# Performance work log

Hardware: AMD Instinct MI355X
Metric: run time of the kernel (lower is better)

Reference implementation:

```python
import jax, jax.numpy as jnp
import numpy as np

BATCH, SEQ, H_IN, N_STATE, H_OUT = 16, 4096, 128, 256, 128
RMIN, RMAX, MAX_PHASE = 0.9, 1.0, 6.283


def setup_inputs() -> dict:
    key = jax.random.key(0)
    ks = jax.random.split(key, 9)
    u = jax.random.normal(ks[0], (BATCH, SEQ, H_IN), jnp.float32)
    # LRU exponential parameterization init (matches torch __init__)
    u1 = jax.random.uniform(ks[1], (N_STATE,), jnp.float32)
    u2 = jax.random.uniform(ks[2], (N_STATE,), jnp.float32)
    nu_log = jnp.log(-0.5 * jnp.log(u1 * (RMAX + RMIN) * (RMAX - RMIN) + RMIN ** 2))
    theta_log = jnp.log(MAX_PHASE * u2)
    lam_abs = jnp.exp(-jnp.exp(nu_log))
    gamma_log = jnp.log(jnp.sqrt(1.0 - lam_abs ** 2))
    s2in = np.sqrt(2.0 * H_IN).astype(np.float32)
    B_re = jax.random.normal(ks[3], (N_STATE, H_IN), jnp.float32) / s2in
    B_im = jax.random.normal(ks[4], (N_STATE, H_IN), jnp.float32) / s2in
    sst = np.sqrt(float(N_STATE)).astype(np.float32)
    C_re = jax.random.normal(ks[5], (H_OUT, N_STATE), jnp.float32) / sst
    C_im = jax.random.normal(ks[6], (H_OUT, N_STATE), jnp.float32) / sst
    D = jax.random.normal(ks[7], (H_OUT, H_IN), jnp.float32) / np.sqrt(float(H_IN)).astype(np.float32)
    return dict(u=u, nu_log=nu_log, theta_log=theta_log, gamma_log=gamma_log,
                B_re=B_re, B_im=B_im, C_re=C_re, C_im=C_im, D=D)


def _combine(a, b):
    # complex affine composition: (l, x) o (l', x') -> (l*l', l'*x + x')
    l1r, l1i, x1r, x1i = a
    l2r, l2i, x2r, x2i = b
    lr = l1r * l2r - l1i * l2i
    li = l1r * l2i + l1i * l2r
    xr = l2r * x1r - l2i * x1i + x2r
    xi = l2r * x1i + l2i * x1r + x2i
    return (lr, li, xr, xi)


def reference(u, nu_log, theta_log, gamma_log, B_re, B_im, C_re, C_im, D):
    lam_mod = jnp.exp(-jnp.exp(nu_log))          # |lambda|, [N]
    th = jnp.exp(theta_log)
    lam_re = lam_mod * jnp.cos(th)
    lam_im = lam_mod * jnp.sin(th)
    gammas = jnp.exp(gamma_log)                  # [N]
    # input projection Bu_t = gamma * (B @ u_t), complex -> real/imag parts
    Bu_re = jnp.einsum('blh,nh->bln', u, B_re) * gammas  # [B,L,N]
    Bu_im = jnp.einsum('blh,nh->bln', u, B_im) * gammas
    Bsz, L, N = Bu_re.shape
    lr = jnp.broadcast_to(lam_re, (Bsz, L, N))
    li = jnp.broadcast_to(lam_im, (Bsz, L, N))
    # parallel scan of x_t = lambda * x_{t-1} + Bu_t, x0 = 0
    _, _, xr, xi = jax.lax.associative_scan(_combine, (lr, li, Bu_re, Bu_im), axis=1)
    zero = jnp.zeros((Bsz, 1, N), u.dtype)
    pre_re = jnp.concatenate([zero, xr[:, :-1]], axis=1)  # states[:, :-1]
    pre_im = jnp.concatenate([zero, xi[:, :-1]], axis=1)
    # y_t = Re(C x_{t-1}) + D u_t
    y = (jnp.einsum('bln,on->blo', pre_re, C_re)
         - jnp.einsum('bln,on->blo', pre_im, C_im)
         + jnp.einsum('blh,oh->blo', u, D))
    return y
```

## Files before the change

kernel.cpp:

```cpp
#include <hip/hip_runtime.h>
#include <math.h>

#define BATCH 16
#define SEQ   4096
#define HIN   128
#define NST   256
#define HOUT  128
#define CL    32
#define NC    (SEQ/CL)
#define ROWS  (BATCH*SEQ)
#define KTOT  640

typedef __attribute__((ext_vector_type(8))) short short8;
typedef __attribute__((ext_vector_type(4))) float f32x4;

__device__ inline unsigned short f2bf(float f) {
  union { float f; unsigned u; } v; v.f = f;
  unsigned r = v.u + 0x7FFFu + ((v.u >> 16) & 1u);
  return (unsigned short)(r >> 16);
}
__device__ inline float bf2f(unsigned short s) {
  union { unsigned u; float f; } v; v.u = ((unsigned)s) << 16;
  return v.f;
}
__device__ inline float bits2f(unsigned u) {
  union { unsigned u; float f; } v; v.u = u; return v.f;
}

__global__ __launch_bounds__(256) void k_prep(
    const float* __restrict__ nu_log, const float* __restrict__ theta_log,
    const float* __restrict__ gamma_log,
    const float* __restrict__ Bre, const float* __restrict__ Bim,
    const float* __restrict__ Cre, const float* __restrict__ Cim,
    const float* __restrict__ Dm,
    float* __restrict__ lamre, float* __restrict__ lamim,
    unsigned short* __restrict__ Wb, unsigned short* __restrict__ W2) {
  int idx = blockIdx.x*256 + threadIdx.x;
  if (idx < NST) {
    float lm = expf(-expf(nu_log[idx]));
    float th = expf(theta_log[idx]);
    lamre[idx] = lm * cosf(th);
    lamim[idx] = lm * sinf(th);
  }
  if (idx < 512*HIN) {
    int r = idx >> 7, h = idx & 127;
    int g = r >> 7;
    int w = r & 127;
    int n = g*64 + (w & 63);
    float gm = expf(gamma_log[n]);
    float v = (w < 64) ? Bre[n*HIN + h] : Bim[n*HIN + h];
    Wb[idx] = f2bf(gm * v);
  }
  if (idx < HOUT*KTOT) {
    int o = idx / KTOT, k = idx - o*KTOT;
    float v;
    if (k < 512) {
      int g = k >> 7, kk = k & 127;
      int n = g*64 + (kk & 63);
      v = (kk < 64) ? Cre[o*NST + n] : -Cim[o*NST + n];
    } else {
      v = Dm[o*HIN + (k - 512)];
    }
    W2[idx] = f2bf(v);
  }
}

union SharedK1 {
  unsigned short B[128][72];
  unsigned short stgb[2][32][136];
};
__global__ __launch_bounds__(256, 4) void k_bu(
    const float* __restrict__ u, const unsigned short* __restrict__ Wb,
    const float* __restrict__ lamre, const float* __restrict__ lamim,
    float* __restrict__ S_re, float* __restrict__ S_im) {
  __shared__ unsigned short Asl[64][136];
  __shared__ SharedK1 sh;
  int tid = threadIdx.x;
  int row0 = blockIdx.x * 64;
  int wid = tid >> 6, lane = tid & 63;
  int lm = lane & 15, lq = lane >> 4;
  int m0 = wid * 16;
  int b = row0 >> 12;
  int cbase = (row0 & 4095) >> 5;
#pragma unroll
  for (int cc = 0; cc < 4; ++cc) {
    int ch = cc*256 + tid;
    int r = ch >> 4, h0 = (ch & 15) * 8;
    const float* src = u + (size_t)(row0 + r)*HIN + h0;
    float4 v0 = *(const float4*)src;
    float4 v1 = *(const float4*)(src + 4);
    unsigned short o[8];
    o[0]=f2bf(v0.x); o[1]=f2bf(v0.y); o[2]=f2bf(v0.z); o[3]=f2bf(v0.w);
    o[4]=f2bf(v1.x); o[5]=f2bf(v1.y); o[6]=f2bf(v1.z); o[7]=f2bf(v1.w);
    *(short8*)&Asl[r][h0] = *(const short8*)o;
  }
  for (int g = 0; g < 4; ++g) {
    f32x4 accB[8];
#pragma unroll
    for (int j = 0; j < 8; ++j) accB[j] = (f32x4)0.f;
    for (int kh = 0; kh < 2; ++kh) {
      __syncthreads();
#pragma unroll
      for (int cc = 0; cc < 4; ++cc) {
        int ch = cc*256 + tid;
        int r = ch >> 3, h0 = (ch & 7) * 8;
        *(short8*)&sh.B[r][h0] = *(const short8*)&Wb[(size_t)(g*128 + r)*HIN + kh*64 + h0];
      }
      __syncthreads();
#pragma unroll
      for (int ks2 = 0; ks2 < 2; ++ks2) {
        int k0 = (kh*2 + ks2)*32 + lq*8;
        short8 a = *(const short8*)&Asl[m0 + lm][k0];
#pragma unroll
        for (int j = 0; j < 8; ++j) {
          short8 bb = *(const short8*)&sh.B[j*16 + lm][k0 - kh*64];
          accB[j] = __builtin_amdgcn_mfma_f32_16x16x32_bf16(a, bb, accB[j], 0, 0, 0);
        }
      }
    }
    __syncthreads();
#pragma unroll
    for (int j = 0; j < 8; ++j)
#pragma unroll
      for (int r = 0; r < 4; ++r) {
        int row = m0 + lq*4 + r;
        sh.stgb[row >> 5][row & 31][j*16 + lm] = f2bf(accB[j][r]);
      }
    __syncthreads();
    if (tid < 128) {
      int buf = tid >> 6, nl = tid & 63;
      int ng = g*64 + nl;
      float lr = lamre[ng], li = lamim[ng];
      float rr[CL], ri[CL];
#pragma unroll
      for (int t = 0; t < CL; ++t) {
        rr[t] = bf2f(sh.stgb[buf][t][nl]);
        ri[t] = bf2f(sh.stgb[buf][t][64 + nl]);
      }
      float sr = 0.f, si = 0.f;
#pragma unroll
      for (int t = 0; t < CL; ++t) {
        float nr = lr*sr - li*si + rr[t];
        float ni = lr*si + li*sr + ri[t];
        sr = nr; si = ni;
      }
      int c = cbase + buf;
      int idx = (b*NC + c)*NST + ng;
      S_re[idx] = sr; S_im[idx] = si;
    }
  }
}

__global__ __launch_bounds__(64) void k_scan(
    const float* __restrict__ S_re, const float* __restrict__ S_im,
    const float* __restrict__ lamre, const float* __restrict__ lamim,
    unsigned* __restrict__ X0Pk) {
  int b = blockIdx.x >> 2;
  int n = (blockIdx.x & 3) * 64 + threadIdx.x;
  float ar = lamre[n], ai = lamim[n];
#pragma unroll
  for (int s = 0; s < 5; ++s) { float nr = ar*ar - ai*ai, ni = 2.f*ar*ai; ar = nr; ai = ni; }
  const float* Sr = S_re + (size_t)b*NC*NST + n;
  const float* Si = S_im + (size_t)b*NC*NST + n;
  unsigned* Xp = X0Pk + (size_t)b*NC*NST + n;
  float Are[16], Aim[16], Bre[16], Bim[16];
#pragma unroll
  for (int cc = 0; cc < 16; ++cc) { Are[cc] = Sr[cc*NST]; Aim[cc] = Si[cc*NST]; }
  float xr = 0.f, xi = 0.f;
#pragma unroll
  for (int seg = 0; seg < 8; ++seg) {
    if (seg < 7) {
      const float* pr = Sr + (size_t)(seg+1)*16*NST;
      const float* pi = Si + (size_t)(seg+1)*16*NST;
      if (seg & 1) {
#pragma unroll
        for (int cc = 0; cc < 16; ++cc) { Are[cc] = pr[cc*NST]; Aim[cc] = pi[cc*NST]; }
      } else {
#pragma unroll
        for (int cc = 0; cc < 16; ++cc) { Bre[cc] = pr[cc*NST]; Bim[cc] = pi[cc*NST]; }
      }
    }
#pragma unroll
    for (int cc = 0; cc < 16; ++cc) {
      Xp[(size_t)(seg*16 + cc)*NST] = ((unsigned)f2bf(xi) << 16) | (unsigned)f2bf(xr);
      float cr = (seg & 1) ? Bre[cc] : Are[cc];
      float ci = (seg & 1) ? Bim[cc] : Aim[cc];
      float nr = ar*xr - ai*xi + cr;
      float ni = ar*xi + ai*xr + ci;
      xr = nr; xi = ni;
    }
  }
}

__global__ __launch_bounds__(256, 2) void k_out3(
    const float* __restrict__ u, const unsigned short* __restrict__ Wb,
    const unsigned short* __restrict__ W2,
    const float* __restrict__ lamre, const float* __restrict__ lamim,
    const unsigned* __restrict__ X0Pk,
    float* __restrict__ y) {
  __shared__ unsigned short Asl[64][136];
  __shared__ unsigned short Bh[128][72];
  __shared__ unsigned short stgb[2][32][136];
  __shared__ unsigned short preS[64][136];
  int tid = threadIdx.x;
  int row0 = blockIdx.x * 64;
  int wid = tid >> 6, lane = tid & 63;
  int lm = lane & 15, lq = lane >> 4;
  int m0 = wid * 16;
  int c0 = row0 >> 5;
#pragma unroll
  for (int cc = 0; cc < 4; ++cc) {
    int ch = cc*256 + tid;
    int r = ch >> 4, h0 = (ch & 15) * 8;
    const float* src = u + (size_t)(row0 + r)*HIN + h0;
    float4 v0 = *(const float4*)src;
    float4 v1 = *(const float4*)(src + 4);
    unsigned short o[8];
    o[0]=f2bf(v0.x); o[1]=f2bf(v0.y); o[2]=f2bf(v0.z); o[3]=f2bf(v0.w);
    o[4]=f2bf(v1.x); o[5]=f2bf(v1.y); o[6]=f2bf(v1.z); o[7]=f2bf(v1.w);
    *(short8*)&Asl[r][h0] = *(const short8*)o;
  }
  f32x4 accY[8];
#pragma unroll
  for (int j = 0; j < 8; ++j) accY[j] = (f32x4)0.f;
  for (int g = 0; g < 4; ++g) {
    f32x4 accB[8];
#pragma unroll
    for (int j = 0; j < 8; ++j) accB[j] = (f32x4)0.f;
    for (int kh = 0; kh < 2; ++kh) {
      __syncthreads();
#pragma unroll
      for (int cc = 0; cc < 4; ++cc) {
        int ch = cc*256 + tid;
        int r = ch >> 3, h0 = (ch & 7) * 8;
        *(short8*)&Bh[r][h0] = *(const short8*)&Wb[(size_t)(g*128 + r)*HIN + kh*64 + h0];
      }
      __syncthreads();
#pragma unroll
      for (int ks2 = 0; ks2 < 2; ++ks2) {
        int k0 = (kh*2 + ks2)*32 + lq*8;
        short8 a = *(const short8*)&Asl[m0 + lm][k0];
#pragma unroll
        for (int j = 0; j < 8; ++j) {
          short8 bb = *(const short8*)&Bh[j*16 + lm][k0 - kh*64];
          accB[j] = __builtin_amdgcn_mfma_f32_16x16x32_bf16(a, bb, accB[j], 0, 0, 0);
        }
      }
    }
#pragma unroll
    for (int j = 0; j < 8; ++j)
#pragma unroll
      for (int r = 0; r < 4; ++r) {
        int row = m0 + lq*4 + r;
        stgb[row >> 5][row & 31][j*16 + lm] = f2bf(accB[j][r]);
      }
    __syncthreads();
    if (tid < 128) {
      int buf = tid >> 6, nl = tid & 63;
      int ng = g*64 + nl;
      float lr = lamre[ng], li = lamim[ng];
      float rr[CL], ri[CL];
#pragma unroll
      for (int t = 0; t < CL; ++t) {
        rr[t] = bf2f(stgb[buf][t][nl]);
        ri[t] = bf2f(stgb[buf][t][64 + nl]);
      }
      unsigned xp = X0Pk[(size_t)(c0 + buf)*NST + ng];
      float sr = bits2f(xp << 16), si = bits2f(xp & 0xFFFF0000u);
#pragma unroll
      for (int t = 0; t < CL; ++t) {
        preS[buf*32 + t][nl]      = f2bf(sr);
        preS[buf*32 + t][64 + nl] = f2bf(si);
        float nr = lr*sr - li*si + rr[t];
        float ni = lr*si + li*sr + ri[t];
        sr = nr; si = ni;
      }
    }
    __syncthreads();
    for (int kh = 0; kh < 2; ++kh) {
      if (kh) __syncthreads();
#pragma unroll
      for (int cc = 0; cc < 4; ++cc) {
        int ch = cc*256 + tid;
        int r = ch >> 3, h0 = (ch & 7) * 8;
        *(short8*)&Bh[r][h0] = *(const short8*)&W2[(size_t)r*KTOT + g*128 + kh*64 + h0];
      }
      __syncthreads();
#pragma unroll
      for (int ks2 = 0; ks2 < 2; ++ks2) {
        int k0 = (kh*2 + ks2)*32 + lq*8;
        short8 a = *(const short8*)&preS[m0 + lm][k0];
#pragma unroll
        for (int j = 0; j < 8; ++j) {
          short8 bb = *(const short8*)&Bh[j*16 + lm][k0 - kh*64];
          accY[j] = __builtin_amdgcn_mfma_f32_16x16x32_bf16(a, bb, accY[j], 0, 0, 0);
        }
      }
    }
  }
  for (int kh = 0; kh < 2; ++kh) {
    __syncthreads();
#pragma unroll
    for (int cc = 0; cc < 4; ++cc) {
      int ch = cc*256 + tid;
      int r = ch >> 3, h0 = (ch & 7) * 8;
      *(short8*)&Bh[r][h0] = *(const short8*)&W2[(size_t)r*KTOT + 512 + kh*64 + h0];
    }
    __syncthreads();
#pragma unroll
    for (int ks2 = 0; ks2 < 2; ++ks2) {
      int k0 = (kh*2 + ks2)*32 + lq*8;
      short8 a = *(const short8*)&Asl[m0 + lm][k0];
#pragma unroll
      for (int j = 0; j < 8; ++j) {
        short8 bb = *(const short8*)&Bh[j*16 + lm][k0 - kh*64];
        accY[j] = __builtin_amdgcn_mfma_f32_16x16x32_bf16(a, bb, accY[j], 0, 0, 0);
      }
    }
  }
#pragma unroll
  for (int j = 0; j < 8; ++j)
#pragma unroll
    for (int r = 0; r < 4; ++r)
      y[(size_t)(row0 + m0 + lq*4 + r)*HOUT + j*16 + lm] = accY[j][r];
}

extern "C" void kernel_launch(void* const* d_in, const int* in_sizes, int n_in,
                              void* d_out, int out_size, void* d_ws, size_t ws_size,
                              hipStream_t stream) {
  const float* u         = (const float*)d_in[0];
  const float* nu_log    = (const float*)d_in[1];
  const float* theta_log = (const float*)d_in[2];
  const float* gamma_log = (const float*)d_in[3];
  const float* B_re      = (const float*)d_in[4];
  const float* B_im      = (const float*)d_in[5];
  const float* C_re      = (const float*)d_in[6];
  const float* C_im      = (const float*)d_in[7];
  const float* Dm        = (const float*)d_in[8];
  float* y = (float*)d_out;
  char* ws = (char*)d_ws;

  size_t off = 0;
  float* lamre = (float*)(ws + off);            off += 1024;
  float* lamim = (float*)(ws + off);            off += 1024;
  unsigned short* Wb = (unsigned short*)(ws + off); off += 131072;
  unsigned short* W2 = (unsigned short*)(ws + off); off += 163840;
  float* S_re = (float*)(ws + off);             off += 2097152;
  float* S_im = (float*)(ws + off);             off += 2097152;
  unsigned* X0Pk = (unsigned*)(ws + off);       off += 2097152;

  k_prep<<<320, 256, 0, stream>>>(nu_log, theta_log, gamma_log, B_re, B_im,
                                  C_re, C_im, Dm, lamre, lamim, Wb, W2);
  k_bu<<<ROWS/64, 256, 0, stream>>>(u, Wb, lamre, lamim, S_re, S_im);
  k_scan<<<64, 64, 0, stream>>>(S_re, S_im, lamre, lamim, X0Pk);
  k_out3<<<ROWS/64, 256, 0, stream>>>(u, Wb, W2, lamre, lamim, X0Pk, y);
}
```

Measured before the change: 174.9 us.

## Load full-K weight tiles at once and overlap W2 load with scan

Both kernels now stage the whole 128-wide K slice of the weight tile in shared memory in one pass instead of two 64-wide halves, which halves the barrier count per group. In k_out3 the scan staging buffer is reused in place for the pre-states, and the idle upper 128 threads load the W2 tile while the lower half runs the sequential scan. This hides the global load behind the scan and removes barriers. The cost is more shared memory per block, and k_bu's occupancy hint drops from 4 to 3.

```diff
diff --git a/kernel.cpp b/kernel.cpp
--- a/kernel.cpp
+++ b/kernel.cpp
@@ -66,10 +66,10 @@
 }
 
 union SharedK1 {
-  unsigned short B[128][72];
-  unsigned short stgb[2][32][136];
+  unsigned short B[128][136];
+  unsigned short stg[64][136];
 };
-__global__ __launch_bounds__(256, 4) void k_bu(
+__global__ __launch_bounds__(256, 3) void k_bu(
     const float* __restrict__ u, const unsigned short* __restrict__ Wb,
     const float* __restrict__ lamre, const float* __restrict__ lamim,
     float* __restrict__ S_re, float* __restrict__ S_im) {
@@ -95,27 +95,25 @@
     *(short8*)&Asl[r][h0] = *(const short8*)o;
   }
   for (int g = 0; g < 4; ++g) {
+    __syncthreads();
+#pragma unroll
+    for (int cc = 0; cc < 8; ++cc) {
+      int ch = cc*256 + tid;
+      int r = ch >> 4, h0 = (ch & 15) * 8;
+      *(short8*)&sh.B[r][h0] = *(const short8*)&Wb[(size_t)(g*128 + r)*HIN + h0];
+    }
+    __syncthreads();
     f32x4 accB[8];
 #pragma unroll
     for (int j = 0; j < 8; ++j) accB[j] = (f32x4)0.f;
-    for (int kh = 0; kh < 2; ++kh) {
-      __syncthreads();
-#pragma unroll
-      for (int cc = 0; cc < 4; ++cc) {
-        int ch = cc*256 + tid;
-        int r = ch >> 3, h0 = (ch & 7) * 8;
-        *(short8*)&sh.B[r][h0] = *(const short8*)&Wb[(size_t)(g*128 + r)*HIN + kh*64 + h0];
-      }
-      __syncthreads();
-#pragma unroll
-      for (int ks2 = 0; ks2 < 2; ++ks2) {
-        int k0 = (kh*2 + ks2)*32 + lq*8;
-        short8 a = *(const short8*)&Asl[m0 + lm][k0];
-#pragma unroll
-        for (int j = 0; j < 8; ++j) {
-          short8 bb = *(const short8*)&sh.B[j*16 + lm][k0 - kh*64];
-          accB[j] = __builtin_amdgcn_mfma_f32_16x16x32_bf16(a, bb, accB[j], 0, 0, 0);
-        }
+#pragma unroll
+    for (int ks = 0; ks < 4; ++ks) {
+      int k0 = ks*32 + lq*8;
+      short8 a = *(const short8*)&Asl[m0 + lm][k0];
+#pragma unroll
+      for (int j = 0; j < 8; ++j) {
+        short8 bb = *(const short8*)&sh.B[j*16 + lm][k0];
+        accB[j] = __builtin_amdgcn_mfma_f32_16x16x32_bf16(a, bb, accB[j], 0, 0, 0);
       }
     }
     __syncthreads();
@@ -124,7 +122,7 @@
 #pragma unroll
       for (int r = 0; r < 4; ++r) {
         int row = m0 + lq*4 + r;
-        sh.stgb[row >> 5][row & 31][j*16 + lm] = f2bf(accB[j][r]);
+        sh.stg[row][j*16 + lm] = f2bf(accB[j][r]);
       }
     __syncthreads();
     if (tid < 128) {
@@ -134,8 +132,8 @@
       float rr[CL], ri[CL];
 #pragma unroll
       for (int t = 0; t < CL; ++t) {
-        rr[t] = bf2f(sh.stgb[buf][t][nl]);
-        ri[t] = bf2f(sh.stgb[buf][t][64 + nl]);
+        rr[t] = bf2f(sh.stg[buf*32 + t][nl]);
+        ri[t] = bf2f(sh.stg[buf*32 + t][64 + nl]);
       }
       float sr = 0.f, si = 0.f;
 #pragma unroll
@@ -199,9 +197,8 @@
     const unsigned* __restrict__ X0Pk,
     float* __restrict__ y) {
   __shared__ unsigned short Asl[64][136];
-  __shared__ unsigned short Bh[128][72];
-  __shared__ unsigned short stgb[2][32][136];
-  __shared__ unsigned short preS[64][136];
+  __shared__ unsigned short Bh[128][136];
+  __shared__ unsigned short stg[64][136];
   int tid = threadIdx.x;
   int row0 = blockIdx.x * 64;
   int wid = tid >> 6, lane = tid & 63;
@@ -224,27 +221,25 @@
 #pragma unroll
   for (int j = 0; j < 8; ++j) accY[j] = (f32x4)0.f;
   for (int g = 0; g < 4; ++g) {
+    __syncthreads();
+#pragma unroll
+    for (int cc = 0; cc < 8; ++cc) {
+      int ch = cc*256 + tid;
+      int r = ch >> 4, h0 = (ch & 15) * 8;
+      *(short8*)&Bh[r][h0] = *(const short8*)&Wb[(size_t)(g*128 + r)*HIN + h0];
+    }
+    __syncthreads();
     f32x4 accB[8];
 #pragma unroll
     for (int j = 0; j < 8; ++j) accB[j] = (f32x4)0.f;
-    for (int kh = 0; kh < 2; ++kh) {
-      __syncthreads();
-#pragma unroll
-      for (int cc = 0; cc < 4; ++cc) {
-        int ch = cc*256 + tid;
-        int r = ch >> 3, h0 = (ch & 7) * 8;
-        *(short8*)&Bh[r][h0] = *(const short8*)&Wb[(size_t)(g*128 + r)*HIN + kh*64 + h0];
-      }
-      __syncthreads();
-#pragma unroll
-      for (int ks2 = 0; ks2 < 2; ++ks2) {
-        int k0 = (kh*2 + ks2)*32 + lq*8;
-        short8 a = *(const short8*)&Asl[m0 + lm][k0];
-#pragma unroll
-        for (int j = 0; j < 8; ++j) {
-          short8 bb = *(const short8*)&Bh[j*16 + lm][k0 - kh*64];
-          accB[j] = __builtin_amdgcn_mfma_f32_16x16x32_bf16(a, bb, accB[j], 0, 0, 0);
-        }
+#pragma unroll
+    for (int ks = 0; ks < 4; ++ks) {
+      int k0 = ks*32 + lq*8;
+      short8 a = *(const short8*)&Asl[m0 + lm][k0];
+#pragma unroll
+      for (int j = 0; j < 8; ++j) {
+        short8 bb = *(const short8*)&Bh[j*16 + lm][k0];
+        accB[j] = __builtin_amdgcn_mfma_f32_16x16x32_bf16(a, bb, accB[j], 0, 0, 0);
       }
     }
 #pragma unroll
@@ -252,7 +247,7 @@
 #pragma unroll
       for (int r = 0; r < 4; ++r) {
         int row = m0 + lq*4 + r;
-        stgb[row >> 5][row & 31][j*16 + lm] = f2bf(accB[j][r]);
+        stg[row][j*16 + lm] = f2bf(accB[j][r]);
       }
     __syncthreads();
     if (tid < 128) {
@@ -262,60 +257,55 @@
       float rr[CL], ri[CL];
 #pragma unroll
       for (int t = 0; t < CL; ++t) {
-        rr[t] = bf2f(stgb[buf][t][nl]);
-        ri[t] = bf2f(stgb[buf][t][64 + nl]);
+        rr[t] = bf2f(stg[buf*32 + t][nl]);
+        ri[t] = bf2f(stg[buf*32 + t][64 + nl]);
       }
       unsigned xp = X0Pk[(size_t)(c0 + buf)*NST + ng];
       float sr = bits2f(xp << 16), si = bits2f(xp & 0xFFFF0000u);
 #pragma unroll
       for (int t = 0; t < CL; ++t) {
-        preS[buf*32 + t][nl]      = f2bf(sr);
-        preS[buf*32 + t][64 + nl] = f2bf(si);
+        stg[buf*32 + t][nl]      = f2bf(sr);
+        stg[buf*32 + t][64 + nl] = f2bf(si);
         float nr = lr*sr - li*si + rr[t];
         float ni = lr*si + li*sr + ri[t];
         sr = nr; si = ni;
       }
-    }
-    __syncthreads();
-    for (int kh = 0; kh < 2; ++kh) {
-      if (kh) __syncthreads();
-#pragma unroll
-      for (int cc = 0; cc < 4; ++cc) {
-        int ch = cc*256 + tid;
-        int r = ch >> 3, h0 = (ch & 7) * 8;
-        *(short8*)&Bh[r][h0] = *(const short8*)&W2[(size_t)r*KTOT + g*128 + kh*64 + h0];
-      }
-      __syncthreads();
-#pragma unroll
-      for (int ks2 = 0; ks2 < 2; ++ks2) {
-        int k0 = (kh*2 + ks2)*32 + lq*8;
-        short8 a = *(const short8*)&preS[m0 + lm][k0];
-#pragma unroll
-        for (int j = 0; j < 8; ++j) {
-          short8 bb = *(const short8*)&Bh[j*16 + lm][k0 - kh*64];
-          accY[j] = __builtin_amdgcn_mfma_f32_16x16x32_bf16(a, bb, accY[j], 0, 0, 0);
-        }
-      }
-    }
-  }
-  for (int kh = 0; kh < 2; ++kh) {
-    __syncthreads();
-#pragma unroll
-    for (int cc = 0; cc < 4; ++cc) {
-      int ch = cc*256 + tid;
-      int r = ch >> 3, h0 = (ch & 7) * 8;
-      *(short8*)&Bh[r][h0] = *(const short8*)&W2[(size_t)r*KTOT + 512 + kh*64 + h0];
-    }
-    __syncthreads();
-#pragma unroll
-    for (int ks2 = 0; ks2 < 2; ++ks2) {
-      int k0 = (kh*2 + ks2)*32 + lq*8;
-      short8 a = *(const short8*)&Asl[m0 + lm][k0];
+    } else {
+#pragma unroll
+      for (int cc = 0; cc < 16; ++cc) {
+        int ch = cc*128 + (tid - 128);
+        int r = ch >> 4, h0 = (ch & 15) * 8;
+        *(short8*)&Bh[r][h0] = *(const short8*)&W2[(size_t)r*KTOT + g*128 + h0];
+      }
+    }
+    __syncthreads();
+#pragma unroll
+    for (int ks = 0; ks < 4; ++ks) {
+      int k0 = ks*32 + lq*8;
+      short8 a = *(const short8*)&stg[m0 + lm][k0];
 #pragma unroll
       for (int j = 0; j < 8; ++j) {
-        short8 bb = *(const short8*)&Bh[j*16 + lm][k0 - kh*64];
+        short8 bb = *(const short8*)&Bh[j*16 + lm][k0];
         accY[j] = __builtin_amdgcn_mfma_f32_16x16x32_bf16(a, bb, accY[j], 0, 0, 0);
       }
+    }
+  }
+  __syncthreads();
+#pragma unroll
+  for (int cc = 0; cc < 8; ++cc) {
+    int ch = cc*256 + tid;
+    int r = ch >> 4, h0 = (ch & 15) * 8;
+    *(short8*)&Bh[r][h0] = *(const short8*)&W2[(size_t)r*KTOT + 512 + h0];
+  }
+  __syncthreads();
+#pragma unroll
+  for (int ks = 0; ks < 4; ++ks) {
+    int k0 = ks*32 + lq*8;
+    short8 a = *(const short8*)&Asl[m0 + lm][k0];
+#pragma unroll
+    for (int j = 0; j < 8; ++j) {
+      short8 bb = *(const short8*)&Bh[j*16 + lm][k0];
+      accY[j] = __builtin_amdgcn_mfma_f32_16x16x32_bf16(a, bb, accY[j], 0, 0, 0);
     }
   }
 #pragma unroll
```

After: 171.9 us. Within noise of the previous version (-1.7%).
